# Optimization experiments

Measured on AMD Instinct MI355X. Metric: run time of the kernel, lower is better.

Reference implementation:

```python
import jax, jax.numpy as jnp
import numpy as np

SIMS = 16
AMP = 1.0  # cfg['attention_amplifier']


def setup_inputs() -> dict:
    key = jax.random.key(0)
    k1, k2, k3 = jax.random.split(key, 3)
    B, F = 32, 2048
    data = jax.random.normal(k1, (B * SIMS, F), dtype=jnp.float32)
    attention = jax.random.normal(k2, (B * SIMS, F), dtype=jnp.float32)
    W = jax.random.normal(k3, (SIMS, 2 * SIMS), dtype=jnp.float32) * (1.0 / np.sqrt(2 * SIMS))
    b = jnp.zeros((SIMS,), dtype=jnp.float32)
    return {"data": data, "attention": attention, "W": W, "b": b}


def reference(data, attention, W, b):
    s = SIMS
    B = data.shape[0] // s
    inputs = data.reshape(B, s, -1)            # [B, s, F]
    attn_in = attention.reshape(B, s, -1)      # [B, s, G]
    # bmm(inputs^T, attention) -> [B, F, G]
    a = jnp.einsum('bsf,bsg->bfg', inputs, attn_in)
    a = jax.nn.log_softmax(a, axis=1)          # log_softmax over F dim (dim=1)
    # bmm(a, attention^T) -> [B, F, s]
    a = jnp.einsum('bfg,bsg->bfs', a, attn_in)
    concat = jnp.concatenate([jnp.swapaxes(a, 1, 2), inputs], axis=1)  # [B, 2s, F]
    concat = jnp.swapaxes(concat, 1, 2).reshape(-1, 2 * s)             # [B*F, 2s]
    gate = jax.nn.sigmoid(concat @ W.T + b)    # [B*F, s]
    # output.t().contiguous().view(data.shape): [s, B*F] row-major -> [B*s, F]
    gate = gate.T.reshape(data.shape)
    return gate * data * AMP
```

## Files before the change

### kernel.cpp

```cpp
#include <hip/hip_runtime.h>
#include <math.h>

#define LOG2E 1.44269504088896340736f
#define LN2   0.69314718055994530942f

typedef _Float16 half8 __attribute__((ext_vector_type(8)));
typedef float f32x4v __attribute__((ext_vector_type(4)));

#define TROW 24

template <bool ATOMIC>
__global__ __launch_bounds__(256, 4) void kA(const float* __restrict__ data,
                                             const float* __restrict__ attn,
                                             float* __restrict__ Lout) {
    __shared__ _Float16 ThL[128 * TROW];
    __shared__ _Float16 TlL[128 * TROW];
    __shared__ _Float16 zeroH[8];
    __shared__ float Lw[4][256];
    const int tid = threadIdx.x;
    const int b = blockIdx.z, fb = blockIdx.y, gs = blockIdx.x;
    const int wave = tid >> 6, lane = tid & 63;
    const int n = lane & 15, q = lane >> 4;
    const int g0 = gs * 256;

    if (tid < 8) zeroH[tid] = (_Float16)0.0f;

    half8 A1[4];
    {
        const float* Ab = data + (size_t)b * 16 * 2048;
        const int frow = fb * 256 + wave * 64;
#pragma unroll
        for (int r = 0; r < 4; ++r) {
            half8 a;
#pragma unroll
            for (int j = 0; j < 8; ++j) {
                const int s = (q & 1) * 8 + j;
                float x = Ab[(size_t)s * 2048 + frow + r * 16 + n];
                _Float16 h = (_Float16)x;
                a[j] = (q < 2) ? h : (_Float16)(x - (float)h);
            }
            A1[r] = a;
        }
    }

    const _Float16* b1base = ThL + (q & 1) * 8;
    const _Float16* b2base = (q < 2) ? (TlL + q * 8) : zeroH;
    const int b2stride = (q < 2) ? TROW : 0;

    const float* Tb = attn + (size_t)b * 16 * 2048 + g0;
    const int gl = tid >> 1;
    const int sh = (tid & 1) * 8;

    for (int p = 0; p < 2; ++p) {
        {
            const int g = p * 128 + gl;
            half8 hv, lv;
#pragma unroll
            for (int j = 0; j < 8; ++j) {
                float x = Tb[(size_t)(sh + j) * 2048 + g] * LOG2E;
                _Float16 h = (_Float16)x;
                hv[j] = h;
                lv[j] = (_Float16)(x - (float)h);
            }
            *(half8*)(ThL + gl * TROW + sh) = hv;
            *(half8*)(TlL + gl * TROW + sh) = lv;
        }
        __syncthreads();

        for (int gt = 0; gt < 8; ++gt) {
            const int gp = gt * 16 + n;
            half8 B1 = *(const half8*)(b1base + gp * TROW);
            half8 B2 = *(const half8*)(b2base + gp * b2stride);
            float s0 = 0.f, s1 = 0.f;
#pragma unroll
            for (int r = 0; r < 4; ++r) {
                f32x4v C = {0.f, 0.f, 0.f, 0.f};
                C = __builtin_amdgcn_mfma_f32_16x16x32_f16(A1[r], B1, C, 0, 0, 0);
                C = __builtin_amdgcn_mfma_f32_16x16x32_f16(A1[r], B2, C, 0, 0, 0);
                float e = __builtin_amdgcn_exp2f(C[0]) + __builtin_amdgcn_exp2f(C[1])
                        + __builtin_amdgcn_exp2f(C[2]) + __builtin_amdgcn_exp2f(C[3]);
                if (r & 1) s1 += e; else s0 += e;
            }
            float sum = s0 + s1;
            sum += __shfl_xor(sum, 16);
            sum += __shfl_xor(sum, 32);
            if (q == 0) Lw[wave][p * 128 + gp] = sum;
        }
        __syncthreads();
    }

    {
        const float v = Lw[0][tid] + Lw[1][tid] + Lw[2][tid] + Lw[3][tid];
        if (ATOMIC)
            atomicAdd(&Lout[(size_t)b * 2048 + g0 + tid], v);
        else
            Lout[((size_t)fb * 32 + b) * 2048 + g0 + tid] = v;
    }
}

#define TP 260
__global__ __launch_bounds__(256) void kTail(const float* __restrict__ attn,
                                             const float* __restrict__ Lpart, int nparts,
                                             float* __restrict__ Mpart,
                                             float* __restrict__ cpart) {
    __shared__ float Tsh[16 * TP];
    __shared__ float Lsh[256];
    __shared__ float red[16][17];
    const int tid = threadIdx.x;
    const int seg = blockIdx.x, b = blockIdx.y;
    const int g0 = seg * 256;

#pragma unroll
    for (int s = 0; s < 16; ++s)
        Tsh[s * TP + tid] = attn[(size_t)(b * 16 + s) * 2048 + g0 + tid];
    {
        float sum = 0.f;
        for (int p = 0; p < nparts; ++p)
            sum += Lpart[((size_t)p * 32 + b) * 2048 + g0 + tid];
        Lsh[tid] = LN2 * __builtin_amdgcn_logf(sum);
    }
    __syncthreads();

    {
        const int t = tid & 15, i = tid >> 4;
        float acc = 0.f;
#pragma unroll
        for (int k = 0; k < 4; ++k) {
            float4 l  = *(const float4*)(Lsh + i * 16 + k * 4);
            float4 tv = *(const float4*)(Tsh + t * TP + i * 16 + k * 4);
            acc += l.x * tv.x + l.y * tv.y + l.z * tv.z + l.w * tv.w;
        }
        red[t][i] = acc;
    }
    __syncthreads();
    if (tid < 16) {
        float s = 0.f;
#pragma unroll
        for (int k = 0; k < 16; ++k) s += red[tid][k];
        cpart[((size_t)seg * 32 + b) * 16 + tid] = s;
    }

    {
        const int s = tid >> 4, t = tid & 15;
        float a0 = 0.f, a1 = 0.f;
#pragma unroll 4
        for (int qk = 0; qk < 32; ++qk) {
            float4 x = *(const float4*)(Tsh + s * TP + qk * 8);
            float4 y = *(const float4*)(Tsh + t * TP + qk * 8);
            a0 += x.x * y.x + x.y * y.y + x.z * y.z + x.w * y.w;
            float4 x2 = *(const float4*)(Tsh + s * TP + qk * 8 + 4);
            float4 y2 = *(const float4*)(Tsh + t * TP + qk * 8 + 4);
            a1 += x2.x * y2.x + x2.y * y2.y + x2.z * y2.z + x2.w * y2.w;
        }
        Mpart[((size_t)seg * 32 + b) * 256 + tid] = a0 + a1;
    }
}

__global__ __launch_bounds__(256) void kC2(const float* __restrict__ data,
                                           const float* __restrict__ Mpart,
                                           const float* __restrict__ cpart,
                                           const float* __restrict__ W,
                                           const float* __restrict__ bias,
                                           float* __restrict__ out) {
    __shared__ float Msh[256];
    __shared__ float csh[16];
    __shared__ float Vsh[256];
    __shared__ float w0sh[16];
    const int tid = threadIdx.x;
    const int b = blockIdx.y;
    const int f = blockIdx.x * 256 + tid;

    {
        float m = 0.f;
#pragma unroll
        for (int p = 0; p < 8; ++p) m += Mpart[((size_t)p * 32 + b) * 256 + tid];
        Msh[tid] = m;
        if (tid < 16) {
            float c = 0.f;
#pragma unroll
            for (int p = 0; p < 8; ++p) c += cpart[((size_t)p * 32 + b) * 16 + tid];
            csh[tid] = c;
        }
    }
    __syncthreads();
    {
        const int s = tid >> 4, j = tid & 15;
        float acc = 0.f;
#pragma unroll
        for (int t = 0; t < 16; ++t) acc += Msh[s * 16 + t] * W[j * 32 + t];
        Vsh[s * 16 + j] = acc + W[j * 32 + 16 + s];
        if (s == 0) {
            float w0 = 0.f;
#pragma unroll
            for (int t = 0; t < 16; ++t) w0 += csh[t] * W[j * 32 + t];
            w0sh[j] = bias[j] - w0;
        }
    }
    __syncthreads();

    float As[16];
#pragma unroll
    for (int s = 0; s < 16; ++s)
        As[s] = data[(size_t)(b * 16 + s) * 2048 + f];
#pragma unroll
    for (int j = 0; j < 16; ++j) {
        float p = w0sh[j];
#pragma unroll
        for (int s = 0; s < 16; ++s) p += As[s] * Vsh[s * 16 + j];
        float e = __builtin_amdgcn_exp2f(-LOG2E * p);
        float gate = __builtin_amdgcn_rcpf(1.0f + e);
        size_t r = (size_t)(j * 32 + b) * 2048 + f;
        out[r] = gate * data[r];
    }
}

extern "C" void kernel_launch(void* const* d_in, const int* in_sizes, int n_in,
                              void* d_out, int out_size, void* d_ws, size_t ws_size,
                              hipStream_t stream) {
    const float* data = (const float*)d_in[0];
    const float* attn = (const float*)d_in[1];
    const float* W    = (const float*)d_in[2];
    const float* bias = (const float*)d_in[3];
    float* out = (float*)d_out;
    float* ws  = (float*)d_ws;

    const size_t LP = 8 * 32 * 2048;
    const size_t need_big = LP + 65536 + 4096;

    if (ws_size >= need_big * sizeof(float)) {
        float* Lpart = ws;
        float* Mpart = ws + LP;
        float* cpart = Mpart + 65536;
        kA<false><<<dim3(8, 8, 32), 256, 0, stream>>>(data, attn, Lpart);
        kTail<<<dim3(8, 32), 256, 0, stream>>>(attn, Lpart, 8, Mpart, cpart);
        kC2<<<dim3(8, 32), 256, 0, stream>>>(data, Mpart, cpart, W, bias, out);
    } else {
        float* Lsum  = ws;
        float* Mpart = ws + 65536;
        float* cpart = Mpart + 65536;
        hipMemsetAsync(Lsum, 0, 65536 * sizeof(float), stream);
        kA<true><<<dim3(8, 8, 32), 256, 0, stream>>>(data, attn, Lsum);
        kTail<<<dim3(8, 32), 256, 0, stream>>>(attn, Lsum, 1, Mpart, cpart);
        kC2<<<dim3(8, 32), 256, 0, stream>>>(data, Mpart, cpart, W, bias, out);
    }
}
```

Measured before the change: 98.95 us.

## Switch logsumexp kernel to 32x32x16 MFMA with split-fp16 three-product accumulation

New measurement: 98.39 us. No clear change (-0.6%).

```diff
diff --git a/kernel.cpp b/kernel.cpp
--- a/kernel.cpp
+++ b/kernel.cpp
@@ -5,7 +5,7 @@
 #define LN2   0.69314718055994530942f
 
 typedef _Float16 half8 __attribute__((ext_vector_type(8)));
-typedef float f32x4v __attribute__((ext_vector_type(4)));
+typedef float f32x16 __attribute__((ext_vector_type(16)));
 
 #define TROW 24
 
@@ -15,37 +15,26 @@
                                              float* __restrict__ Lout) {
     __shared__ _Float16 ThL[128 * TROW];
     __shared__ _Float16 TlL[128 * TROW];
-    __shared__ _Float16 zeroH[8];
     __shared__ float Lw[4][256];
     const int tid = threadIdx.x;
     const int b = blockIdx.z, fb = blockIdx.y, gs = blockIdx.x;
     const int wave = tid >> 6, lane = tid & 63;
-    const int n = lane & 15, q = lane >> 4;
+    const int n = lane & 31;
+    const int q = lane >> 5;
     const int g0 = gs * 256;
 
-    if (tid < 8) zeroH[tid] = (_Float16)0.0f;
-
-    half8 A1[4];
+    half8 Ah, Al;
     {
         const float* Ab = data + (size_t)b * 16 * 2048;
-        const int frow = fb * 256 + wave * 64;
-#pragma unroll
-        for (int r = 0; r < 4; ++r) {
-            half8 a;
-#pragma unroll
-            for (int j = 0; j < 8; ++j) {
-                const int s = (q & 1) * 8 + j;
-                float x = Ab[(size_t)s * 2048 + frow + r * 16 + n];
-                _Float16 h = (_Float16)x;
-                a[j] = (q < 2) ? h : (_Float16)(x - (float)h);
-            }
-            A1[r] = a;
-        }
-    }
-
-    const _Float16* b1base = ThL + (q & 1) * 8;
-    const _Float16* b2base = (q < 2) ? (TlL + q * 8) : zeroH;
-    const int b2stride = (q < 2) ? TROW : 0;
+        const int frow = fb * 128 + wave * 32;
+#pragma unroll
+        for (int j = 0; j < 8; ++j) {
+            float x = Ab[(size_t)(q * 8 + j) * 2048 + frow + n];
+            _Float16 h = (_Float16)x;
+            Ah[j] = h;
+            Al[j] = (_Float16)(x - (float)h);
+        }
+    }
 
     const float* Tb = attn + (size_t)b * 16 * 2048 + g0;
     const int gl = tid >> 1;
@@ -67,24 +56,29 @@
         }
         __syncthreads();
 
-        for (int gt = 0; gt < 8; ++gt) {
-            const int gp = gt * 16 + n;
-            half8 B1 = *(const half8*)(b1base + gp * TROW);
-            half8 B2 = *(const half8*)(b2base + gp * b2stride);
-            float s0 = 0.f, s1 = 0.f;
-#pragma unroll
-            for (int r = 0; r < 4; ++r) {
-                f32x4v C = {0.f, 0.f, 0.f, 0.f};
-                C = __builtin_amdgcn_mfma_f32_16x16x32_f16(A1[r], B1, C, 0, 0, 0);
-                C = __builtin_amdgcn_mfma_f32_16x16x32_f16(A1[r], B2, C, 0, 0, 0);
-                float e = __builtin_amdgcn_exp2f(C[0]) + __builtin_amdgcn_exp2f(C[1])
-                        + __builtin_amdgcn_exp2f(C[2]) + __builtin_amdgcn_exp2f(C[3]);
-                if (r & 1) s1 += e; else s0 += e;
+#pragma unroll
+        for (int gt = 0; gt < 4; ++gt) {
+            const int gp = gt * 32 + n;
+            half8 Bh = *(const half8*)(ThL + gp * TROW + q * 8);
+            half8 Bl = *(const half8*)(TlL + gp * TROW + q * 8);
+
+            f32x16 C = {0.f, 0.f, 0.f, 0.f, 0.f, 0.f, 0.f, 0.f,
+                        0.f, 0.f, 0.f, 0.f, 0.f, 0.f, 0.f, 0.f};
+            C = __builtin_amdgcn_mfma_f32_32x32x16_f16(Ah, Bh, C, 0, 0, 0);
+            C = __builtin_amdgcn_mfma_f32_32x32x16_f16(Al, Bh, C, 0, 0, 0);
+            C = __builtin_amdgcn_mfma_f32_32x32x16_f16(Ah, Bl, C, 0, 0, 0);
+
+            float s0 = 0.f, s1 = 0.f, s2 = 0.f, s3 = 0.f;
+#pragma unroll
+            for (int i = 0; i < 4; ++i) {
+                s0 += __builtin_amdgcn_exp2f(C[4 * i + 0]);
+                s1 += __builtin_amdgcn_exp2f(C[4 * i + 1]);
+                s2 += __builtin_amdgcn_exp2f(C[4 * i + 2]);
+                s3 += __builtin_amdgcn_exp2f(C[4 * i + 3]);
             }
-            float sum = s0 + s1;
-            sum += __shfl_xor(sum, 16);
+            float sum = (s0 + s1) + (s2 + s3);
             sum += __shfl_xor(sum, 32);
-            if (q == 0) Lw[wave][p * 128 + gp] = sum;
+            if (lane < 32) Lw[wave][p * 128 + gt * 32 + n] = sum;
         }
         __syncthreads();
     }
@@ -224,22 +218,22 @@
     float* out = (float*)d_out;
     float* ws  = (float*)d_ws;
 
-    const size_t LP = 8 * 32 * 2048;
+    const size_t LP = 16 * 32 * 2048;
     const size_t need_big = LP + 65536 + 4096;
 
     if (ws_size >= need_big * sizeof(float)) {
         float* Lpart = ws;
         float* Mpart = ws + LP;
         float* cpart = Mpart + 65536;
-        kA<false><<<dim3(8, 8, 32), 256, 0, stream>>>(data, attn, Lpart);
-        kTail<<<dim3(8, 32), 256, 0, stream>>>(attn, Lpart, 8, Mpart, cpart);
+        kA<false><<<dim3(8, 16, 32), 256, 0, stream>>>(data, attn, Lpart);
+        kTail<<<dim3(8, 32), 256, 0, stream>>>(attn, Lpart, 16, Mpart, cpart);
         kC2<<<dim3(8, 32), 256, 0, stream>>>(data, Mpart, cpart, W, bias, out);
     } else {
         float* Lsum  = ws;
         float* Mpart = ws + 65536;
         float* cpart = Mpart + 65536;
         hipMemsetAsync(Lsum, 0, 65536 * sizeof(float), stream);
-        kA<true><<<dim3(8, 8, 32), 256, 0, stream>>>(data, attn, Lsum);
+        kA<true><<<dim3(8, 16, 32), 256, 0, stream>>>(data, attn, Lsum);
         kTail<<<dim3(8, 32), 256, 0, stream>>>(attn, Lsum, 1, Mpart, cpart);
         kC2<<<dim3(8, 32), 256, 0, stream>>>(data, Mpart, cpart, W, bias, out);
     }
```
